# Optimization experiments

Hardware: AMD Instinct MI355X
Metric: run time of the kernel (lower is better)

## Reference

```python
import jax, jax.numpy as jnp
import numpy as np


def setup_inputs() -> dict:
    key = jax.random.key(0)
    k1, k2, k3, k4 = jax.random.split(key, 4)
    B, Sq, Sk, d = 16, 2048, 2048, 64
    queries = jax.random.normal(k1, (B, Sq, d), dtype=jnp.float32)
    keys = jax.random.normal(k2, (B, Sk, d), dtype=jnp.float32)
    values = jax.random.normal(k3, (B, Sk, d), dtype=jnp.float32)
    # True = padded key position (masked out)
    key_padding_mask = jax.random.randint(k4, (B, Sk), 0, 2) == 1
    return {"queries": queries, "keys": keys, "values": values,
            "key_padding_mask": key_padding_mask}


def reference(queries, keys, values, key_padding_mask):
    d = queries.shape[-1]
    # scores: [B, Sq, Sk]
    scores = jnp.einsum("bqd,bkd->bqk", queries, keys) / jnp.sqrt(
        jnp.asarray(d, dtype=queries.dtype))
    # padded keys get -inf before softmax (mask broadcast over query dim)
    scores = jnp.where(key_padding_mask[:, None, :], -jnp.inf, scores)
    attention_weights = jax.nn.softmax(scores, axis=2)
    return jnp.einsum("bqk,bkd->bqd", attention_weights, values)
```

## Files before the change

kernel.cpp:

```cpp
#include <hip/hip_runtime.h>
#include <hip/hip_bf16.h>

#define NB 16
#define SQ 2048
#define SK 2048
#define DH 64
#define RS 72
#define NKT (SK / 64)

#define KBLK 1024
#define VBLK 512
#define BBLK 128

typedef __attribute__((ext_vector_type(8))) short short8;
typedef __attribute__((ext_vector_type(8))) __bf16 bf16x8;
typedef __attribute__((ext_vector_type(4))) float floatx4;
typedef __attribute__((ext_vector_type(2))) unsigned uint2v;

__device__ __forceinline__ unsigned pk2(float a, float b) {
  __hip_bfloat162 h = __float22bfloat162_rn(make_float2(a, b));
  unsigned u; __builtin_memcpy(&u, &h, 4); return u;
}
__device__ __forceinline__ floatx4 mfma16(short8 a, short8 b, floatx4 c) {
  return __builtin_amdgcn_mfma_f32_16x16x32_bf16(
      __builtin_bit_cast(bf16x8, a), __builtin_bit_cast(bf16x8, b), c, 0, 0, 0);
}

__global__ __launch_bounds__(256)
void prepass(const float* __restrict__ K, const float* __restrict__ V,
             const int* __restrict__ m, short* __restrict__ Kb,
             short* __restrict__ Vt, float* __restrict__ bias) {
  __shared__ unsigned tlw[64 * 33];
  const int blk = blockIdx.x;
  const int t = threadIdx.x;
  if (blk < KBLK) {
    size_t i8 = ((size_t)blk * 256 + t) * 8;
    floatx4 a = *(const floatx4*)(K + i8);
    floatx4 b = *(const floatx4*)(K + i8 + 4);
    union { unsigned u[4]; short8 s; } w;
    w.u[0] = pk2(a[0], a[1]); w.u[1] = pk2(a[2], a[3]);
    w.u[2] = pk2(b[0], b[1]); w.u[3] = pk2(b[2], b[3]);
    *(short8*)(Kb + i8) = w.s;
  } else if (blk < KBLK + VBLK) {
    const int bt = blk - KBLK;
    const int key2 = t & 31;
    const int dg = (t >> 5) * 8;
    const float* vp0 = V + ((size_t)bt * 64 + 2 * key2) * 64 + dg;
    const float* vp1 = vp0 + 64;
    floatx4 va  = *(const floatx4*)(vp0);
    floatx4 va2 = *(const floatx4*)(vp0 + 4);
    floatx4 vb  = *(const floatx4*)(vp1);
    floatx4 vb2 = *(const floatx4*)(vp1 + 4);
#pragma unroll
    for (int j = 0; j < 4; ++j) {
      tlw[(dg + j) * 33 + key2]     = pk2(va[j],  vb[j]);
      tlw[(dg + 4 + j) * 33 + key2] = pk2(va2[j], vb2[j]);
    }
    __syncthreads();
    const short* tls = (const short*)tlw;
    short* dst = Vt + (size_t)bt * 4096;
#pragma unroll
    for (int i = 0; i < 2; ++i) {
      int idx = i * 2048 + t * 8;
      int d = idx >> 6, key = idx & 63;
      *(short8*)(dst + idx) = *(const short8*)(tls + d * 66 + key);
    }
  } else {
    int i = (blk - KBLK - VBLK) * 256 + t;
    bias[i] = m[i] ? -1e30f : 0.0f;
  }
}

__global__ __launch_bounds__(256)
void attn_main(const float* __restrict__ Q, const short* __restrict__ Kb,
               const short* __restrict__ Vt, const float* __restrict__ bias,
               float* __restrict__ Out, float* __restrict__ Op1,
               float2* __restrict__ ml) {
  __shared__ __align__(16) short ks[64 * RS];
  __shared__ __align__(16) short vt[64 * RS];
  __shared__ __align__(16) short pb[4 * 16 * RS];

  const int half = blockIdx.x >> 9;
  const int rest = blockIdx.x & 511;
  const int b    = rest >> 5;
  const int qt   = rest & 31;
  const int tid  = threadIdx.x;
  const int lane = tid & 63;
  const int wave = tid >> 6;
  const int L    = lane & 15;
  const int quad = lane >> 4;
  const int q0w  = qt * 64 + wave * 16;
  const int kt0  = half << 4;

  const float QS = 0.125f * 1.4426950408889634f;
  short8 qf[2];
  {
    const float* qp = Q + ((size_t)b * SQ + q0w + L) * DH + 8 * quad;
#pragma unroll
    for (int c = 0; c < 2; ++c) {
      floatx4 a  = *(const floatx4*)(qp + 32 * c);
      floatx4 a2 = *(const floatx4*)(qp + 32 * c + 4);
      union { unsigned u[4]; short8 s; } w;
      w.u[0] = pk2(a[0] * QS, a[1] * QS);
      w.u[1] = pk2(a[2] * QS, a[3] * QS);
      w.u[2] = pk2(a2[0] * QS, a2[1] * QS);
      w.u[3] = pk2(a2[2] * QS, a2[3] * QS);
      qf[c] = w.s;
    }
  }

  floatx4 o[4];
#pragma unroll
  for (int n = 0; n < 4; ++n) o[n] = (floatx4){0.f, 0.f, 0.f, 0.f};
  float m_q = -1e30f, l_q = 0.f;

  short* pbw = pb + wave * 16 * RS;

  const short* kg = Kb + (size_t)b * SK * DH;
  const short* vg = Vt + (size_t)b * 32 * 4096;
  const float* bg = bias + b * SK;

  const int srow = tid >> 3;
  const int scol = (tid & 7) * 8;

  short8 kr[2], vr[2];
#pragma unroll
  for (int i = 0; i < 2; ++i) {
    kr[i] = *(const short8*)(kg + (size_t)kt0 * 4096 + i * 2048 + tid * 8);
    vr[i] = *(const short8*)(vg + (size_t)kt0 * 4096 + i * 2048 + tid * 8);
  }

  for (int kt = kt0; kt < kt0 + 16; ++kt) {
#pragma unroll
    for (int i = 0; i < 2; ++i) {
      int row = i * 32 + srow;
      *(short8*)(ks + row * RS + scol) = kr[i];
      *(short8*)(vt + row * RS + scol) = vr[i];
    }
    __syncthreads();

    if (kt + 1 < kt0 + 16) {
      const short* kn = kg + (size_t)(kt + 1) * 4096;
      const short* vn = vg + (size_t)(kt + 1) * 4096;
#pragma unroll
      for (int i = 0; i < 2; ++i) {
        kr[i] = *(const short8*)(kn + i * 2048 + tid * 8);
        vr[i] = *(const short8*)(vn + i * 2048 + tid * 8);
      }
    }

    floatx4 s[4];
#pragma unroll
    for (int t = 0; t < 4; ++t) {
      short8 kf0 = *(short8*)(ks + (16 * t + L) * RS + quad * 8);
      short8 kf1 = *(short8*)(ks + (16 * t + L) * RS + 32 + quad * 8);
      floatx4 z = (floatx4){0.f, 0.f, 0.f, 0.f};
      s[t] = mfma16(kf0, qf[0], z);
      s[t] = mfma16(kf1, qf[1], s[t]);
    }

    const float* bq = bg + kt * 64 + 4 * quad;
    float a[4][4];
    float rm = -1e30f;
#pragma unroll
    for (int t = 0; t < 4; ++t) {
      floatx4 bv = *(const floatx4*)(bq + 16 * t);
#pragma unroll
      for (int r = 0; r < 4; ++r) {
        a[t][r] = s[t][r] + bv[r];
        rm = fmaxf(rm, a[t][r]);
      }
    }
    rm = fmaxf(rm, __shfl_xor(rm, 16));
    rm = fmaxf(rm, __shfl_xor(rm, 32));
    float mn = fmaxf(m_q, rm);
    float alpha_q = __builtin_amdgcn_exp2f(m_q - mn);
    m_q = mn;

    float rs = 0.f;
#pragma unroll
    for (int t = 0; t < 4; ++t) {
      float p0 = __builtin_amdgcn_exp2f(a[t][0] - mn);
      float p1 = __builtin_amdgcn_exp2f(a[t][1] - mn);
      float p2 = __builtin_amdgcn_exp2f(a[t][2] - mn);
      float p3 = __builtin_amdgcn_exp2f(a[t][3] - mn);
      rs += (p0 + p1) + (p2 + p3);
      uint2v w; w.x = pk2(p0, p1); w.y = pk2(p2, p3);
      *(uint2v*)(pbw + L * RS + 16 * t + 4 * quad) = w;
    }
    rs += __shfl_xor(rs, 16);
    rs += __shfl_xor(rs, 32);
    l_q = alpha_q * l_q + rs;

    float av[4];
#pragma unroll
    for (int r = 0; r < 4; ++r) av[r] = __shfl(alpha_q, quad * 4 + r);
#pragma unroll
    for (int n = 0; n < 4; ++n)
#pragma unroll
      for (int r = 0; r < 4; ++r) o[n][r] *= av[r];

    short8 pf0 = *(short8*)(pbw + L * RS + quad * 8);
    short8 pf1 = *(short8*)(pbw + L * RS + 32 + quad * 8);

#pragma unroll
    for (int n = 0; n < 4; ++n) {
      short8 vf0 = *(short8*)(vt + (16 * n + L) * RS + quad * 8);
      short8 vf1 = *(short8*)(vt + (16 * n + L) * RS + 32 + quad * 8);
      o[n] = mfma16(pf0, vf0, o[n]);
      o[n] = mfma16(pf1, vf1, o[n]);
    }
    __syncthreads();
  }

  float* Od = half ? Op1 : Out;
#pragma unroll
  for (int r = 0; r < 4; ++r) {
    size_t row = (size_t)b * SQ + q0w + quad * 4 + r;
#pragma unroll
    for (int n = 0; n < 4; ++n)
      Od[row * DH + 16 * n + L] = o[n][r];
  }
  if (lane < 16)
    ml[((size_t)half * NB + b) * SQ + q0w + lane] = make_float2(m_q, l_q);
}

__global__ __launch_bounds__(256)
void combine(const float* __restrict__ Op1, const float2* __restrict__ ml,
             float* __restrict__ Out) {
  int idx = blockIdx.x * 256 + threadIdx.x;
  int q = idx >> 3;
  int dc = (idx & 7) * 8;
  float2 s0 = ml[q];
  float2 s1 = ml[NB * SQ + q];
  float M = fmaxf(s0.x, s1.x);
  float w0 = __builtin_amdgcn_exp2f(s0.x - M);
  float w1 = __builtin_amdgcn_exp2f(s1.x - M);
  float inv = 1.0f / (s0.y * w0 + s1.y * w1);
  const float* p0 = Out + (size_t)q * DH + dc;
  const float* p1 = Op1 + (size_t)q * DH + dc;
  floatx4 a0 = *(const floatx4*)(p0);
  floatx4 a1 = *(const floatx4*)(p0 + 4);
  floatx4 b0 = *(const floatx4*)(p1);
  floatx4 b1 = *(const floatx4*)(p1 + 4);
  floatx4 r0 = (a0 * w0 + b0 * w1) * inv;
  floatx4 r1 = (a1 * w0 + b1 * w1) * inv;
  *(floatx4*)(Out + (size_t)q * DH + dc) = r0;
  *(floatx4*)(Out + (size_t)q * DH + dc + 4) = r1;
}

extern "C" void kernel_launch(void* const* d_in, const int* in_sizes, int n_in,
                              void* d_out, int out_size, void* d_ws, size_t ws_size,
                              hipStream_t stream) {
  const float* Q = (const float*)d_in[0];
  const float* K = (const float*)d_in[1];
  const float* V = (const float*)d_in[2];
  const int* mask = (const int*)d_in[3];
  float* Out = (float*)d_out;

  char* ws = (char*)d_ws;
  short*  Kb   = (short*)(ws);
  short*  Vt   = (short*)(ws + 4194304);
  float*  bias = (float*)(ws + 8388608);
  float2* ml   = (float2*)(ws + 8519680);
  float*  Op1  = (float*)(ws + 9043968);

  prepass  <<<KBLK + VBLK + BBLK, 256, 0, stream>>>(K, V, mask, Kb, Vt, bias);
  attn_main<<<2 * NB * (SQ / 64), 256, 0, stream>>>(Q, Kb, Vt, bias, Out, Op1, ml);
  combine  <<<NB * SQ * DH / 8 / 256, 256, 0, stream>>>(Op1, ml, Out);
}
```

Measured before the change: 126.1 us.

## Switch attention to 32x32x16 MFMA with 128-query tiles and XOR-swizzled LDS

Each wave now owns 32 query rows instead of 16 and uses the 32x32x16 bf16 MFMA, so every block covers 128 queries and the grid is halved. The row padding in shared memory is replaced by an XOR swizzle of the 8-element chunks, which shrinks LDS per tile. The output rescale is skipped when no lane's running max increased, and the output stores become 16-byte vector writes. This doubles K/V tile reuse per block and lowers LDS traffic per MFMA, at the cost of more registers per thread and fewer blocks in flight (512 in total).

```diff
diff --git a/kernel.cpp b/kernel.cpp
--- a/kernel.cpp
+++ b/kernel.cpp
@@ -5,8 +5,6 @@
 #define SQ 2048
 #define SK 2048
 #define DH 64
-#define RS 72
-#define NKT (SK / 64)
 
 #define KBLK 1024
 #define VBLK 512
@@ -15,14 +13,15 @@
 typedef __attribute__((ext_vector_type(8))) short short8;
 typedef __attribute__((ext_vector_type(8))) __bf16 bf16x8;
 typedef __attribute__((ext_vector_type(4))) float floatx4;
+typedef __attribute__((ext_vector_type(16))) float floatx16;
 typedef __attribute__((ext_vector_type(2))) unsigned uint2v;
 
 __device__ __forceinline__ unsigned pk2(float a, float b) {
   __hip_bfloat162 h = __float22bfloat162_rn(make_float2(a, b));
   unsigned u; __builtin_memcpy(&u, &h, 4); return u;
 }
-__device__ __forceinline__ floatx4 mfma16(short8 a, short8 b, floatx4 c) {
-  return __builtin_amdgcn_mfma_f32_16x16x32_bf16(
+__device__ __forceinline__ floatx16 mfma32(short8 a, short8 b, floatx16 c) {
+  return __builtin_amdgcn_mfma_f32_32x32x16_bf16(
       __builtin_bit_cast(bf16x8, a), __builtin_bit_cast(bf16x8, b), c, 0, 0, 0);
 }
 
@@ -76,30 +75,31 @@
                const short* __restrict__ Vt, const float* __restrict__ bias,
                float* __restrict__ Out, float* __restrict__ Op1,
                float2* __restrict__ ml) {
-  __shared__ __align__(16) short ks[64 * RS];
-  __shared__ __align__(16) short vt[64 * RS];
-  __shared__ __align__(16) short pb[4 * 16 * RS];
-
-  const int half = blockIdx.x >> 9;
-  const int rest = blockIdx.x & 511;
-  const int b    = rest >> 5;
-  const int qt   = rest & 31;
+  __shared__ __align__(16) short ks[64 * 64];
+  __shared__ __align__(16) short vt[64 * 64];
+  __shared__ __align__(16) short pb[4 * 32 * 64];
+
+  const int half = blockIdx.x >> 8;
+  const int rest = blockIdx.x & 255;
+  const int b    = rest >> 4;
+  const int qt   = rest & 15;
   const int tid  = threadIdx.x;
+  const int wave = tid >> 6;
   const int lane = tid & 63;
-  const int wave = tid >> 6;
-  const int L    = lane & 15;
-  const int quad = lane >> 4;
-  const int q0w  = qt * 64 + wave * 16;
+  const int n32  = lane & 31;
+  const int h    = lane >> 5;
+  const int sw   = n32 & 7;
+  const int q0   = qt * 128 + wave * 32;
   const int kt0  = half << 4;
 
   const float QS = 0.125f * 1.4426950408889634f;
-  short8 qf[2];
+  short8 qf[4];
   {
-    const float* qp = Q + ((size_t)b * SQ + q0w + L) * DH + 8 * quad;
-#pragma unroll
-    for (int c = 0; c < 2; ++c) {
-      floatx4 a  = *(const floatx4*)(qp + 32 * c);
-      floatx4 a2 = *(const floatx4*)(qp + 32 * c + 4);
+    const float* qp = Q + ((size_t)b * SQ + q0 + n32) * DH + 8 * h;
+#pragma unroll
+    for (int c = 0; c < 4; ++c) {
+      floatx4 a  = *(const floatx4*)(qp + 16 * c);
+      floatx4 a2 = *(const floatx4*)(qp + 16 * c + 4);
       union { unsigned u[4]; short8 s; } w;
       w.u[0] = pk2(a[0] * QS, a[1] * QS);
       w.u[1] = pk2(a[2] * QS, a[3] * QS);
@@ -109,120 +109,126 @@
     }
   }
 
-  floatx4 o[4];
-#pragma unroll
-  for (int n = 0; n < 4; ++n) o[n] = (floatx4){0.f, 0.f, 0.f, 0.f};
+  floatx16 o0, o1;
+#pragma unroll
+  for (int i = 0; i < 16; ++i) { o0[i] = 0.f; o1[i] = 0.f; }
   float m_q = -1e30f, l_q = 0.f;
 
-  short* pbw = pb + wave * 16 * RS;
+  short* pw = pb + wave * 2048;
 
   const short* kg = Kb + (size_t)b * SK * DH;
   const short* vg = Vt + (size_t)b * 32 * 4096;
   const float* bg = bias + b * SK;
 
-  const int srow = tid >> 3;
-  const int scol = (tid & 7) * 8;
+  const int srow  = tid >> 3;
+  const int schk  = tid & 7;
+  const int sphys = schk ^ (srow & 7);
+  const int soff0 = srow * 64 + sphys * 8;
+  const int soff1 = (srow + 32) * 64 + sphys * 8;
+  const int goff0 = srow * 64 + schk * 8;
+  const int goff1 = (srow + 32) * 64 + schk * 8;
 
   short8 kr[2], vr[2];
-#pragma unroll
-  for (int i = 0; i < 2; ++i) {
-    kr[i] = *(const short8*)(kg + (size_t)kt0 * 4096 + i * 2048 + tid * 8);
-    vr[i] = *(const short8*)(vg + (size_t)kt0 * 4096 + i * 2048 + tid * 8);
+  {
+    const short* kn = kg + (size_t)kt0 * 4096;
+    const short* vn = vg + (size_t)kt0 * 4096;
+    kr[0] = *(const short8*)(kn + goff0); kr[1] = *(const short8*)(kn + goff1);
+    vr[0] = *(const short8*)(vn + goff0); vr[1] = *(const short8*)(vn + goff1);
   }
 
   for (int kt = kt0; kt < kt0 + 16; ++kt) {
-#pragma unroll
-    for (int i = 0; i < 2; ++i) {
-      int row = i * 32 + srow;
-      *(short8*)(ks + row * RS + scol) = kr[i];
-      *(short8*)(vt + row * RS + scol) = vr[i];
-    }
+    *(short8*)(ks + soff0) = kr[0]; *(short8*)(ks + soff1) = kr[1];
+    *(short8*)(vt + soff0) = vr[0]; *(short8*)(vt + soff1) = vr[1];
     __syncthreads();
 
     if (kt + 1 < kt0 + 16) {
       const short* kn = kg + (size_t)(kt + 1) * 4096;
       const short* vn = vg + (size_t)(kt + 1) * 4096;
-#pragma unroll
-      for (int i = 0; i < 2; ++i) {
-        kr[i] = *(const short8*)(kn + i * 2048 + tid * 8);
-        vr[i] = *(const short8*)(vn + i * 2048 + tid * 8);
+      kr[0] = *(const short8*)(kn + goff0); kr[1] = *(const short8*)(kn + goff1);
+      vr[0] = *(const short8*)(vn + goff0); vr[1] = *(const short8*)(vn + goff1);
+    }
+
+    floatx16 s0, s1;
+#pragma unroll
+    for (int i = 0; i < 16; ++i) { s0[i] = 0.f; s1[i] = 0.f; }
+#pragma unroll
+    for (int c = 0; c < 4; ++c) {
+      short8 kf0 = *(short8*)(ks + n32 * 64        + ((2 * c + h) ^ sw) * 8);
+      short8 kf1 = *(short8*)(ks + (32 + n32) * 64 + ((2 * c + h) ^ sw) * 8);
+      s0 = mfma32(kf0, qf[c], s0);
+      s1 = mfma32(kf1, qf[c], s1);
+    }
+
+    const float* bq = bg + kt * 64;
+    float sc0[16], sc1[16];
+    float rm = -1e30f;
+#pragma unroll
+    for (int u = 0; u < 4; ++u) {
+      floatx4 bv0 = *(const floatx4*)(bq + 8 * u + 4 * h);
+      floatx4 bv1 = *(const floatx4*)(bq + 32 + 8 * u + 4 * h);
+#pragma unroll
+      for (int i = 0; i < 4; ++i) {
+        sc0[4 * u + i] = s0[4 * u + i] + bv0[i];
+        sc1[4 * u + i] = s1[4 * u + i] + bv1[i];
+        rm = fmaxf(rm, fmaxf(sc0[4 * u + i], sc1[4 * u + i]));
       }
     }
-
-    floatx4 s[4];
-#pragma unroll
-    for (int t = 0; t < 4; ++t) {
-      short8 kf0 = *(short8*)(ks + (16 * t + L) * RS + quad * 8);
-      short8 kf1 = *(short8*)(ks + (16 * t + L) * RS + 32 + quad * 8);
-      floatx4 z = (floatx4){0.f, 0.f, 0.f, 0.f};
-      s[t] = mfma16(kf0, qf[0], z);
-      s[t] = mfma16(kf1, qf[1], s[t]);
-    }
-
-    const float* bq = bg + kt * 64 + 4 * quad;
-    float a[4][4];
-    float rm = -1e30f;
-#pragma unroll
-    for (int t = 0; t < 4; ++t) {
-      floatx4 bv = *(const floatx4*)(bq + 16 * t);
-#pragma unroll
-      for (int r = 0; r < 4; ++r) {
-        a[t][r] = s[t][r] + bv[r];
-        rm = fmaxf(rm, a[t][r]);
-      }
-    }
-    rm = fmaxf(rm, __shfl_xor(rm, 16));
     rm = fmaxf(rm, __shfl_xor(rm, 32));
     float mn = fmaxf(m_q, rm);
-    float alpha_q = __builtin_amdgcn_exp2f(m_q - mn);
+    float alpha = __builtin_amdgcn_exp2f(m_q - mn);
+    bool up = mn > m_q;
     m_q = mn;
 
     float rs = 0.f;
 #pragma unroll
-    for (int t = 0; t < 4; ++t) {
-      float p0 = __builtin_amdgcn_exp2f(a[t][0] - mn);
-      float p1 = __builtin_amdgcn_exp2f(a[t][1] - mn);
-      float p2 = __builtin_amdgcn_exp2f(a[t][2] - mn);
-      float p3 = __builtin_amdgcn_exp2f(a[t][3] - mn);
+    for (int u = 0; u < 4; ++u) {
+      float p0 = __builtin_amdgcn_exp2f(sc0[4 * u + 0] - mn);
+      float p1 = __builtin_amdgcn_exp2f(sc0[4 * u + 1] - mn);
+      float p2 = __builtin_amdgcn_exp2f(sc0[4 * u + 2] - mn);
+      float p3 = __builtin_amdgcn_exp2f(sc0[4 * u + 3] - mn);
       rs += (p0 + p1) + (p2 + p3);
       uint2v w; w.x = pk2(p0, p1); w.y = pk2(p2, p3);
-      *(uint2v*)(pbw + L * RS + 16 * t + 4 * quad) = w;
-    }
-    rs += __shfl_xor(rs, 16);
+      *(uint2v*)(pw + n32 * 64 + (u ^ sw) * 8 + 4 * h) = w;
+
+      float q0v = __builtin_amdgcn_exp2f(sc1[4 * u + 0] - mn);
+      float q1v = __builtin_amdgcn_exp2f(sc1[4 * u + 1] - mn);
+      float q2v = __builtin_amdgcn_exp2f(sc1[4 * u + 2] - mn);
+      float q3v = __builtin_amdgcn_exp2f(sc1[4 * u + 3] - mn);
+      rs += (q0v + q1v) + (q2v + q3v);
+      uint2v w2; w2.x = pk2(q0v, q1v); w2.y = pk2(q2v, q3v);
+      *(uint2v*)(pw + n32 * 64 + ((4 + u) ^ sw) * 8 + 4 * h) = w2;
+    }
     rs += __shfl_xor(rs, 32);
-    l_q = alpha_q * l_q + rs;
-
-    float av[4];
-#pragma unroll
-    for (int r = 0; r < 4; ++r) av[r] = __shfl(alpha_q, quad * 4 + r);
-#pragma unroll
-    for (int n = 0; n < 4; ++n)
-#pragma unroll
-      for (int r = 0; r < 4; ++r) o[n][r] *= av[r];
-
-    short8 pf0 = *(short8*)(pbw + L * RS + quad * 8);
-    short8 pf1 = *(short8*)(pbw + L * RS + 32 + quad * 8);
-
-#pragma unroll
-    for (int n = 0; n < 4; ++n) {
-      short8 vf0 = *(short8*)(vt + (16 * n + L) * RS + quad * 8);
-      short8 vf1 = *(short8*)(vt + (16 * n + L) * RS + 32 + quad * 8);
-      o[n] = mfma16(pf0, vf0, o[n]);
-      o[n] = mfma16(pf1, vf1, o[n]);
+    l_q = alpha * l_q + rs;
+
+    if (__ballot(up)) {
+#pragma unroll
+      for (int i = 0; i < 16; ++i) { o0[i] *= alpha; o1[i] *= alpha; }
+    }
+
+#pragma unroll
+    for (int c = 0; c < 4; ++c) {
+      short8 pf  = *(short8*)(pw + n32 * 64 + ((2 * c + h) ^ sw) * 8);
+      short8 vf0 = *(short8*)(vt + n32 * 64        + ((2 * c + h) ^ sw) * 8);
+      short8 vf1 = *(short8*)(vt + (32 + n32) * 64 + ((2 * c + h) ^ sw) * 8);
+      o0 = mfma32(vf0, pf, o0);
+      o1 = mfma32(vf1, pf, o1);
     }
     __syncthreads();
   }
 
   float* Od = half ? Op1 : Out;
-#pragma unroll
-  for (int r = 0; r < 4; ++r) {
-    size_t row = (size_t)b * SQ + q0w + quad * 4 + r;
-#pragma unroll
-    for (int n = 0; n < 4; ++n)
-      Od[row * DH + 16 * n + L] = o[n][r];
-  }
-  if (lane < 16)
-    ml[((size_t)half * NB + b) * SQ + q0w + lane] = make_float2(m_q, l_q);
+  float* orow = Od + ((size_t)b * SQ + q0 + n32) * DH;
+#pragma unroll
+  for (int u = 0; u < 4; ++u) {
+    floatx4 w0, w1;
+#pragma unroll
+    for (int i = 0; i < 4; ++i) { w0[i] = o0[4 * u + i]; w1[i] = o1[4 * u + i]; }
+    *(floatx4*)(orow + 8 * u + 4 * h)      = w0;
+    *(floatx4*)(orow + 32 + 8 * u + 4 * h) = w1;
+  }
+  if (lane < 32)
+    ml[(size_t)half * NB * SQ + (size_t)b * SQ + q0 + lane] = make_float2(m_q, l_q);
 }
 
 __global__ __launch_bounds__(256)
@@ -266,6 +272,6 @@
   float*  Op1  = (float*)(ws + 9043968);
 
   prepass  <<<KBLK + VBLK + BBLK, 256, 0, stream>>>(K, V, mask, Kb, Vt, bias);
-  attn_main<<<2 * NB * (SQ / 64), 256, 0, stream>>>(Q, Kb, Vt, bias, Out, Op1, ml);
+  attn_main<<<2 * NB * (SQ / 128), 256, 0, stream>>>(Q, Kb, Vt, bias, Out, Op1, ml);
   combine  <<<NB * SQ * DH / 8 / 256, 256, 0, stream>>>(Op1, ml, Out);
 }
```

Measured after the change: 121.1 us. -4.0%, faster.
